# Performance work log

Measured on AMD Instinct MI355X. Metric: run time of the kernel, lower is better.

## Reference

```python
import jax, jax.numpy as jnp
import numpy as np

IOU_HI = 0.5
IOU_LO = 0.0
ROI_BS = 256
POS_RATIO = 0.25
BG = 20  # background class id; valid classes 0..BG-1
NUM_POS = int(ROI_BS * POS_RATIO)
DELTAS_SCALING = np.array([10.0, 10.0, 5.0, 5.0], dtype=np.float32)  # (x, y, w, h)


def _make_boxes(key, shape):
    ka, kb = jax.random.split(key)
    c = jax.random.uniform(ka, shape + (2,), minval=0.05, maxval=0.95)
    s = jax.random.uniform(kb, shape + (2,), minval=0.02, maxval=0.4)
    lo = jnp.clip(c - s / 2, 0.0, 1.0)
    hi = jnp.clip(c + s / 2, 0.0, 1.0)
    return jnp.concatenate([lo, hi], -1)  # (y1, x1, y2, x2), normalized


def setup_inputs() -> dict:
    key = jax.random.key(0)
    k1, k2, k3 = jax.random.split(key, 3)
    B, N, G = 32, 12000, 200
    rois = _make_boxes(k1, (B, N))
    gt_boxes = _make_boxes(k2, (B, G))
    # class == BG marks a padded / invalid GT box
    gt_class_ids = jax.random.randint(k3, (B, G), 0, BG + 1).astype(jnp.int32)
    return {"rois": rois, "gt_class_ids": gt_class_ids, "gt_boxes": gt_boxes}


def _iou(rois, gts):
    # rois [N,4], gts [G,4] in (y1,x1,y2,x2) -> [N,G]
    y1 = jnp.maximum(rois[:, None, 0], gts[None, :, 0])
    x1 = jnp.maximum(rois[:, None, 1], gts[None, :, 1])
    y2 = jnp.minimum(rois[:, None, 2], gts[None, :, 2])
    x2 = jnp.minimum(rois[:, None, 3], gts[None, :, 3])
    inter = jnp.clip(y2 - y1, 0.0) * jnp.clip(x2 - x1, 0.0)
    ar = (rois[:, 2] - rois[:, 0]) * (rois[:, 3] - rois[:, 1])
    ag = (gts[:, 2] - gts[:, 0]) * (gts[:, 3] - gts[:, 1])
    return inter / (ar[:, None] + ag[None, :] - inter + 1e-8)


def _encode(r, g):
    # (tx, ty, tw, th) * scaling, r/g: [K,4] in (y1,x1,y2,x2)
    eps = 1e-6
    rh = r[:, 2] - r[:, 0]; rw = r[:, 3] - r[:, 1]
    rcy = r[:, 0] + rh / 2; rcx = r[:, 1] + rw / 2
    gh = g[:, 2] - g[:, 0]; gw = g[:, 3] - g[:, 1]
    gcy = g[:, 0] + gh / 2; gcx = g[:, 1] + gw / 2
    tx = (gcx - rcx) / (rw + eps)
    ty = (gcy - rcy) / (rh + eps)
    tw = jnp.log(jnp.maximum(gw, eps) / (rw + eps))
    th = jnp.log(jnp.maximum(gh, eps) / (rh + eps))
    return jnp.stack([tx, ty, tw, th], -1) * jnp.asarray(DELTAS_SCALING)


def _per_image(rois, gt_cls, gt_boxes):
    iou = _iou(rois, gt_boxes)                       # [N,G]
    valid_gt = gt_cls < BG
    iou = jnp.where(valid_gt[None, :], iou, -1.0)
    max_iou = iou.max(1)                             # [N]
    best_gt = iou.argmax(1)                          # [N]
    pos = max_iou >= IOU_HI
    neg = (max_iou < IOU_HI) & (max_iou >= IOU_LO)

    # deterministic sampling: highest-IoU positives / negatives first
    pos_val, pos_idx = jax.lax.top_k(jnp.where(pos, max_iou, -1.0), NUM_POS)
    pos_ok = pos_val > 0.0
    neg_val, neg_idx = jax.lax.top_k(jnp.where(neg, max_iou + 2.0, -1.0), ROI_BS)
    neg_ok = neg_val > 0.0

    rP = jnp.arange(NUM_POS, dtype=jnp.float32)
    rN = jnp.arange(ROI_BS, dtype=jnp.float32)
    prio = jnp.concatenate([jnp.where(pos_ok, 1e9 - rP, -1e9 - rP),
                            jnp.where(neg_ok, 1e6 - rN, -1e6 - rN)])
    cand_idx = jnp.concatenate([pos_idx, neg_idx])
    cand_pos = jnp.concatenate([pos_ok, jnp.zeros(ROI_BS, bool)])
    _, sel = jax.lax.top_k(prio, ROI_BS)
    sel_roi = cand_idx[sel]                          # [ROI_BS]
    sel_is_pos = cand_pos[sel]                       # [ROI_BS]

    labels = jnp.where(sel_is_pos, gt_cls[best_gt[sel_roi]], BG)
    rois_sel = rois[sel_roi]                         # [ROI_BS,4]
    gts_sel = gt_boxes[best_gt[sel_roi]]             # [ROI_BS,4]
    t = _encode(rois_sel, gts_sel) * sel_is_pos[:, None].astype(rois.dtype)

    cls_onehot = jax.nn.one_hot(labels, BG + 1, dtype=rois.dtype)   # [ROI_BS,BG+1]
    onehot_fg = jax.nn.one_hot(labels, BG, dtype=rois.dtype)        # zero row for bg
    mask4 = jnp.repeat(onehot_fg, 4, axis=1)                        # [ROI_BS,4*BG]
    deltas_full = (onehot_fg[:, :, None] * t[:, None, :]).reshape(ROI_BS, 4 * BG)
    reg = jnp.concatenate([mask4, deltas_full], -1)                 # [ROI_BS,8*BG]
    return rois_sel, cls_onehot, reg


def reference(rois, gt_class_ids, gt_boxes):
    return jax.vmap(_per_image)(rois, gt_class_ids, gt_boxes)
```

## Files before the change

### kernel.cpp

```cpp
#include <hip/hip_runtime.h>
#include <stdint.h>

#pragma clang fp contract(off)

#define BATCH 32
#define NROI  12000
#define NGT   200
#define BGCLS 20
#define ROIBS 256
#define NPOS  64
#define NBIN  1024
#define CAP   2048
#define TSEL  1024
#define VPT2  12
#define HSH   16
#define HST   (NBIN + 2)
#define DELTA 1e-6f
#define RPT   2
#define IOBLK (256 * RPT)

__device__ __forceinline__ void roi_maxiou_all(const float4* cbox, const float* carea,
                                               int nv, float ry1, float rx1,
                                               float ry2, float rx2,
                                               float& best, int& bj) {
#pragma clang fp contract(off)
  float ar = (ry2 - ry1) * (rx2 - rx1);
  best = -1.0f; bj = 0;
#pragma unroll 4
  for (int j = 0; j < nv; ++j) {
    float4 q = cbox[j];
    float yy1 = fmaxf(ry1, q.x);
    float xx1 = fmaxf(rx1, q.y);
    float yy2 = fminf(ry2, q.z);
    float xx2 = fminf(rx2, q.w);
    float inter = fmaxf(yy2 - yy1, 0.0f) * fmaxf(xx2 - xx1, 0.0f);
    float den = ((ar + carea[j]) - inter) + 1e-8f;
    float iou = inter / den;
    if (iou > best) { best = iou; bj = j; }
  }
}

__device__ __forceinline__ float approx_max(const float4* cbox, const float* carea,
                                            int nv, float4 r) {
  float ar = (r.z - r.x) * (r.w - r.y);
  float va = -1.0f, vb = -1.0f;
#pragma unroll 4
  for (int j = 0; j < nv; ++j) {
    float4 q = cbox[j];
    float yy1 = fmaxf(r.x, q.x);
    float xx1 = fmaxf(r.y, q.y);
    float yy2 = fminf(r.z, q.z);
    float xx2 = fminf(r.w, q.w);
    float inter = fmaxf(yy2 - yy1, 0.0f) * fmaxf(xx2 - xx1, 0.0f);
    float den = ((ar + carea[j]) - inter) + 1e-8f;
    float a = inter * __builtin_amdgcn_rcpf(den);
    if (j & 1) vb = fmaxf(vb, a); else va = fmaxf(va, a);
  }
  return fmaxf(va, vb);
}

template <int NTHR>
__device__ __forceinline__ int stage_gt(float4* cbox, float* carea, int* ccls,
                                        int* snv, int* wtmp,
                                        const float* gtb, const int* gtc, int b) {
  const int tid = threadIdx.x;
  bool valid = false; float4 p = make_float4(0.f, 0.f, 0.f, 0.f); int cls = BGCLS;
  if (tid < NGT) {
    p = *(const float4*)(gtb + ((size_t)b * NGT + tid) * 4);
    cls = gtc[(size_t)b * NGT + tid];
    valid = (cls < BGCLS);
  }
  unsigned long long m = __ballot(valid);
  int w = tid >> 6;
  if ((tid & 63) == 0) wtmp[w] = __popcll(m);
  __syncthreads();
  if (tid == 0) {
    int s = 0;
    for (int i = 0; i < NTHR / 64; ++i) s += wtmp[i];
    *snv = s;
  }
  if (valid) {
    int off = 0;
    for (int i = 0; i < w; ++i) off += wtmp[i];
    int pos = off + __popcll(m & ((1ull << (tid & 63)) - 1ull));
    cbox[pos] = p;
    if (carea) carea[pos] = (p.z - p.x) * (p.w - p.y);
    if (ccls) ccls[pos] = cls;
  }
  __syncthreads();
  return *snv;
}

__global__ __launch_bounds__(256, 3) void k_ioumax(const float* __restrict__ rois,
                                                   const int* __restrict__ gtc,
                                                   const float* __restrict__ gtb,
                                                   float* __restrict__ max_iou) {
#pragma clang fp contract(off)
  __shared__ float4 cbox[NGT];
  __shared__ int snv, wtmp[4];
  const int b = blockIdx.y;
  const int tid = threadIdx.x;
  const int nv = stage_gt<256>(cbox, nullptr, nullptr, &snv, wtmp, gtb, gtc, b);

  const int n0 = blockIdx.x * IOBLK + tid;
  const int n1 = n0 + 256;
  const float4 r0 = (n0 < NROI)
      ? *(const float4*)(rois + ((size_t)b * NROI + n0) * 4)
      : make_float4(2.f, 2.f, 2.f, 2.f);
  const float4 r1 = (n1 < NROI)
      ? *(const float4*)(rois + ((size_t)b * NROI + n1) * 4)
      : make_float4(2.f, 2.f, 2.f, 2.f);
  const float ar0 = (r0.z - r0.x) * (r0.w - r0.y);
  const float ar1 = (r1.z - r1.x) * (r1.w - r1.y);
  float va0 = -1.0f, vb0 = -1.0f, va1 = -1.0f, vb1 = -1.0f;
#pragma unroll 4
  for (int j = 0; j < nv; ++j) {
    float4 q = cbox[j];
    float ag = (q.z - q.x) * (q.w - q.y);
    {
      float yy1 = fmaxf(r0.x, q.x);
      float xx1 = fmaxf(r0.y, q.y);
      float yy2 = fminf(r0.z, q.z);
      float xx2 = fminf(r0.w, q.w);
      float inter = fmaxf(yy2 - yy1, 0.0f) * fmaxf(xx2 - xx1, 0.0f);
      float den = ((ar0 + ag) - inter) + 1e-8f;
      float a = inter * __builtin_amdgcn_rcpf(den);
      if (j & 1) vb0 = fmaxf(vb0, a); else va0 = fmaxf(va0, a);
    }
    {
      float yy1 = fmaxf(r1.x, q.x);
      float xx1 = fmaxf(r1.y, q.y);
      float yy2 = fminf(r1.z, q.z);
      float xx2 = fminf(r1.w, q.w);
      float inter = fmaxf(yy2 - yy1, 0.0f) * fmaxf(xx2 - xx1, 0.0f);
      float den = ((ar1 + ag) - inter) + 1e-8f;
      float a = inter * __builtin_amdgcn_rcpf(den);
      if (j & 1) vb1 = fmaxf(vb1, a); else va1 = fmaxf(va1, a);
    }
  }
  if (n0 < NROI) max_iou[(size_t)b * NROI + n0] = fmaxf(va0, vb0);
  if (n1 < NROI) max_iou[(size_t)b * NROI + n1] = fmaxf(va1, vb1);
}

__global__ __launch_bounds__(TSEL) void k_selA(const float* __restrict__ rois,
                                               const int* __restrict__ gtc,
                                               const float* __restrict__ gtb,
                                               const float* __restrict__ mi,
                                               int* __restrict__ posCnt,
                                               int* __restrict__ posN,
                                               int* __restrict__ posBJ,
                                               int* __restrict__ negCnt,
                                               int* __restrict__ negN,
                                               int* __restrict__ negBJ) {
#pragma clang fp contract(off)
  __shared__ float4 cbox[NGT];
  __shared__ float carea[NGT];
  __shared__ int snv, wtmp[16];
  __shared__ int wtot[16], wnext[16];
  __shared__ int plist[CAP];
  __shared__ unsigned long long keyl[CAP];
  __shared__ int bjl[CAP];
  __shared__ int hs[HSH][HST];
  __shared__ int ss[NBIN];
  __shared__ int scnt, sX, sT, sOk;
  const int b = blockIdx.x >> 1;
  const bool isPos = (blockIdx.x & 1) == 0;
  const int tid = threadIdx.x;
  const int lane = tid & 63;
  const int nv = stage_gt<TSEL>(cbox, carea, nullptr, &snv, wtmp, gtb, gtc, b);

  float v[VPT2];
#pragma unroll
  for (int i = 0; i < VPT2; ++i) {
    int n = tid + (i << 10);
    v[i] = (n < NROI) ? mi[(size_t)b * NROI + n] : -3.0f;
  }

  auto mkbin = [](unsigned kh, unsigned base, int shift) -> int {
    int bin = ((int)(kh - base)) >> shift;
    return max(min(bin, NBIN - 1), 0);
  };
  const unsigned base = isPos ? 0x3F000000u : 0x40000000u;
  const int shift = isPos ? 13 : 11;

  for (int i = tid; i < HSH * HST; i += TSEL) ((int*)hs)[i] = 0;
  if (tid == 0) { scnt = 0; sX = 0; sOk = 0; }
  __syncthreads();
  const int sh = tid & (HSH - 1);
#pragma unroll
  for (int i = 0; i < VPT2; ++i) {
    int n = tid + (i << 10);
    float x = v[i];
    bool inb = isPos ? ((n < NROI) && (x >= 0.5f - DELTA))
                     : ((n < NROI) && (x < 0.5f + DELTA));
    if (inb) {
      unsigned kh = __float_as_uint(isPos ? x : (x + 2.0f));
      atomicAdd(&hs[sh][mkbin(kh, base, shift)], 1);
    }
    bool bnd = (n < NROI) && (x >= 0.5f - DELTA) && (x < 0.5f + DELTA);
    unsigned long long mx = __ballot(bnd);
    if (lane == 0 && mx) atomicAdd(&sX, __popcll(mx));
  }
  __syncthreads();
  const int limitWant = isPos ? NPOS : ROIBS;
  const int needv = limitWant + sX;

  {
    if (tid == 0) sT = 0;
    __syncthreads();
    int cnt_bin = 0;
#pragma unroll
    for (int i = 0; i < HSH; ++i) cnt_bin += hs[i][tid];
    const int w = tid >> 6;
    int sfx = cnt_bin;
#pragma unroll
    for (int off = 1; off < 64; off <<= 1) {
      int t = __shfl_down(sfx, off, 64);
      sfx += (lane + off < 64) ? t : 0;
    }
    if (lane == 0) wtot[w] = sfx;
    __syncthreads();
    if (tid < 16) {
      int s = 0;
      for (int i = tid + 1; i < 16; ++i) s += wtot[i];
      wnext[tid] = s;
    }
    __syncthreads();
    const int suffix = sfx + wnext[w];
    ss[tid] = suffix;
    __syncthreads();
    int nxt = (tid + 1 < NBIN) ? ss[tid + 1] : 0;
    if (suffix >= needv && nxt < needv) sT = tid;
    __syncthreads();
  }
  const int Tc = max(sT - 2, 0);

#pragma unroll
  for (int i = 0; i < VPT2; ++i) {
    int n = tid + (i << 10);
    float x = v[i];
    bool inb = isPos ? ((n < NROI) && (x >= 0.5f - DELTA))
                     : ((n < NROI) && (x < 0.5f + DELTA));
    bool pred = inb &&
        (mkbin(__float_as_uint(isPos ? x : (x + 2.0f)), base, shift) >= Tc);
    unsigned long long mk = __ballot(pred);
    int c = __popcll(mk);
    int bs = 0;
    if (lane == 0 && c) bs = atomicAdd(&scnt, c);
    bs = __shfl(bs, 0, 64);
    if (pred) {
      int idx = bs + __popcll(mk & ((1ull << lane) - 1ull));
      if (idx < CAP) plist[idx] = n;
    }
  }
  __syncthreads();
  const int cnt = min(scnt, CAP);

  for (int i = tid; i < cnt; i += TSEL) {
    int n = plist[i];
    const float4 r = *(const float4*)(rois + ((size_t)b * NROI + n) * 4);
    float best; int bj;
    roi_maxiou_all(cbox, carea, nv, r.x, r.y, r.z, r.w, best, bj);
    bool ok = isPos ? (best >= 0.5f) : (best < 0.5f);
    unsigned kh = __float_as_uint(isPos ? best : (best + 2.0f));
    keyl[i] = ok ? (((unsigned long long)kh << 32) | (unsigned)(0x7fffffff - n))
                 : 0ull;
    bjl[i] = bj;
    if (ok) atomicAdd(&sOk, 1);
  }
  __syncthreads();
  const int limit = min(sOk, limitWant);
  if (tid == 0) { if (isPos) posCnt[b] = limit; else negCnt[b] = limit; }

  int* dstN = isPos ? (posN + (size_t)b * NPOS) : (negN + (size_t)b * ROIBS);
  int* dstB = isPos ? (posBJ + (size_t)b * NPOS) : (negBJ + (size_t)b * ROIBS);
  for (int i = tid; i < cnt; i += TSEL) {
    unsigned long long ki = keyl[i];
    if (ki) {
      int r0 = 0, r1 = 0, r2 = 0, r3 = 0;
      int j = 0;
      for (; j + 4 <= cnt; j += 4) {
        r0 += (keyl[j + 0] > ki);
        r1 += (keyl[j + 1] > ki);
        r2 += (keyl[j + 2] > ki);
        r3 += (keyl[j + 3] > ki);
      }
      for (; j < cnt; ++j) r0 += (keyl[j] > ki);
      int rank = r0 + r1 + r2 + r3;
      if (rank < limit) {
        dstN[rank] = 0x7fffffff - (int)(ki & 0xffffffffu);
        dstB[rank] = bjl[i];
      }
    }
  }
}

__global__ __launch_bounds__(TSEL) void k_emit(const float* __restrict__ rois,
                                               const int* __restrict__ gtc,
                                               const float* __restrict__ gtb,
                                               const int* __restrict__ posCnt,
                                               const int* __restrict__ posN,
                                               const int* __restrict__ posBJ,
                                               const int* __restrict__ negCnt,
                                               const int* __restrict__ negN,
                                               const int* __restrict__ negBJ,
                                               float* __restrict__ out) {
#pragma clang fp contract(off)
  __shared__ float4 cbox[NGT];
  __shared__ float carea[NGT];
  __shared__ int ccls[NGT];
  __shared__ int snv, wtmp[16];
  const int b = blockIdx.x;
  const int tid = threadIdx.x;
  stage_gt<TSEL>(cbox, carea, ccls, &snv, wtmp, gtb, gtc, b);

  const int P = min(posCnt[b], NPOS);
  const int NC = negCnt[b];
  const int slot = tid >> 2, q = tid & 3;
  int r = 0, bj = 0, isp = 0;
  if (slot < P) {
    r = posN[(size_t)b * NPOS + slot];
    bj = posBJ[(size_t)b * NPOS + slot];
    isp = 1;
  } else {
    int j = slot - P;
    if (j < NC) {
      r = negN[(size_t)b * ROIBS + j];
      bj = negBJ[(size_t)b * ROIBS + j];
    }
  }
  const float4 rv = *(const float4*)(rois + ((size_t)b * NROI + r) * 4);
  float ry1 = rv.x, rx1 = rv.y, ry2 = rv.z, rx2 = rv.w;
  int label = isp ? ccls[bj] : BGCLS;

  float* out1 = out;
  float* out2 = out + (size_t)BATCH * ROIBS * 4;
  float* out3 = out + (size_t)BATCH * ROIBS * 25;
  size_t row = (size_t)b * ROIBS + slot;

  if (q == 0) {
    *(float4*)(out1 + row * 4) = rv;
    float* o2 = out2 + row * 21;
    for (int c = 0; c <= BGCLS; ++c) o2[c] = (c == label) ? 1.0f : 0.0f;
  }

  float t0 = 0.f, t1 = 0.f, t2 = 0.f, t3 = 0.f;
  if (isp) {
    const float eps = 1e-6f;
    float4 g = cbox[bj];
    float rh = ry2 - ry1, rw = rx2 - rx1;
    float rcy = ry1 + rh * 0.5f, rcx = rx1 + rw * 0.5f;
    float gh = g.z - g.x, gw = g.w - g.y;
    float gcy = g.x + gh * 0.5f, gcx = g.y + gw * 0.5f;
    t0 = ((gcx - rcx) / (rw + eps)) * 10.0f;
    t1 = ((gcy - rcy) / (rh + eps)) * 10.0f;
    t2 = logf(fmaxf(gw, eps) / (rw + eps)) * 5.0f;
    t3 = logf(fmaxf(gh, eps) / (rh + eps)) * 5.0f;
  }
  int m0 = label * 4;
  float* o3 = out3 + row * 160;
  for (int c = q * 10; c < q * 10 + 10; ++c) {
    float4 wv = make_float4(0.f, 0.f, 0.f, 0.f);
    if (isp) {
      float* wp = &wv.x;
#pragma unroll
      for (int jj = 0; jj < 4; ++jj) {
        int e = c * 4 + jj;
        float x = 0.f;
        if (e >= m0 && e < m0 + 4) x = 1.0f;
        int d = e - 80 - m0;
        if (d == 0) x = t0; else if (d == 1) x = t1;
        else if (d == 2) x = t2; else if (d == 3) x = t3;
        wp[jj] = x;
      }
    }
    *(float4*)(o3 + c * 4) = wv;
  }
}

__global__ __launch_bounds__(TSEL) void k_sel_mono(const float* __restrict__ rois,
                                                   const int* __restrict__ gtc,
                                                   const float* __restrict__ gtb,
                                                   float* __restrict__ out) {
#pragma clang fp contract(off)
  __shared__ float4 cbox[NGT];
  __shared__ float carea[NGT];
  __shared__ int ccls[NGT];
  __shared__ int snv, wtmp[16];
  __shared__ int wtot[16], wnext[16];
  __shared__ int plist[CAP];
  __shared__ unsigned long long keyl[CAP];
  __shared__ int bjl[CAP];
  __shared__ int hs[HSH][HST];
  __shared__ int ss[NBIN];
  __shared__ int sel_r[ROIBS];
  __shared__ int sel_b[ROIBS];
  __shared__ int scnt, sX, sT, sPos;
  const int b = blockIdx.x;
  const int tid = threadIdx.x;
  const int lane = tid & 63;
  if (tid < ROIBS) { sel_r[tid] = 0; sel_b[tid] = 0; }
  const int nv = stage_gt<TSEL>(cbox, carea, ccls, &snv, wtmp, gtb, gtc, b);

  float v[VPT2];
#pragma unroll
  for (int i = 0; i < VPT2; ++i) {
    int n = tid + (i << 10);
    if (n < NROI) {
      const float4 r = *(const float4*)(rois + ((size_t)b * NROI + n) * 4);
      v[i] = approx_max(cbox, carea, nv, r);
    } else v[i] = -3.0f;
  }

  auto mkbin = [](unsigned kh, unsigned base, int shift) -> int {
    int bin = ((int)(kh - base)) >> shift;
    return max(min(bin, NBIN - 1), 0);
  };
  auto find_T = [&](int needv) -> int {
    if (tid == 0) sT = 0;
    __syncthreads();
    int cnt_bin = 0;
#pragma unroll
    for (int i = 0; i < HSH; ++i) cnt_bin += hs[i][tid];
    const int w = tid >> 6;
    int sfx = cnt_bin;
#pragma unroll
    for (int off = 1; off < 64; off <<= 1) {
      int t = __shfl_down(sfx, off, 64);
      sfx += (lane + off < 64) ? t : 0;
    }
    if (lane == 0) wtot[w] = sfx;
    __syncthreads();
    if (tid < 16) {
      int s = 0;
      for (int i = tid + 1; i < 16; ++i) s += wtot[i];
      wnext[tid] = s;
    }
    __syncthreads();
    const int suffix = sfx + wnext[w];
    ss[tid] = suffix;
    __syncthreads();
    int nxt = (tid + 1 < NBIN) ? ss[tid + 1] : 0;
    if (suffix >= needv && nxt < needv) sT = tid;
    __syncthreads();
    return sT;
  };
  auto rank_of = [&](unsigned long long ki, int cnt) -> int {
    int r0 = 0, r1 = 0, r2 = 0, r3 = 0;
    int j = 0;
    for (; j + 4 <= cnt; j += 4) {
      r0 += (keyl[j + 0] > ki);
      r1 += (keyl[j + 1] > ki);
      r2 += (keyl[j + 2] > ki);
      r3 += (keyl[j + 3] > ki);
    }
    for (; j < cnt; ++j) r0 += (keyl[j] > ki);
    return r0 + r1 + r2 + r3;
  };
  const int sh = tid & (HSH - 1);

  for (int i = tid; i < HSH * HST; i += TSEL) ((int*)hs)[i] = 0;
  if (tid == 0) { scnt = 0; sX = 0; sPos = 0; }
  __syncthreads();
#pragma unroll
  for (int i = 0; i < VPT2; ++i) {
    int n = tid + (i << 10);
    float x = v[i];
    bool inb = (n < NROI) && (x >= 0.5f - DELTA);
    if (inb) atomicAdd(&hs[sh][mkbin(__float_as_uint(x), 0x3F000000u, 13)], 1);
    bool bnd = inb && (x < 0.5f + DELTA);
    unsigned long long mx = __ballot(bnd);
    if (lane == 0 && mx) atomicAdd(&sX, __popcll(mx));
  }
  __syncthreads();
  const int XB = sX;
  const int Tp = max(find_T(NPOS + XB) - 2, 0);
#pragma unroll
  for (int i = 0; i < VPT2; ++i) {
    int n = tid + (i << 10);
    float x = v[i];
    bool pred = (n < NROI) && (x >= 0.5f - DELTA) &&
                (mkbin(__float_as_uint(x), 0x3F000000u, 13) >= Tp);
    unsigned long long mk = __ballot(pred);
    int c = __popcll(mk);
    int bs = 0;
    if (lane == 0 && c) bs = atomicAdd(&scnt, c);
    bs = __shfl(bs, 0, 64);
    if (pred) {
      int idx = bs + __popcll(mk & ((1ull << lane) - 1ull));
      if (idx < CAP) plist[idx] = n;
    }
  }
  __syncthreads();
  const int cntp = min(scnt, CAP);
  for (int i = tid; i < cntp; i += TSEL) {
    int n = plist[i];
    const float4 r = *(const float4*)(rois + ((size_t)b * NROI + n) * 4);
    float best; int bj;
    roi_maxiou_all(cbox, carea, nv, r.x, r.y, r.z, r.w, best, bj);
    bool ok = (best >= 0.5f);
    keyl[i] = ok ? (((unsigned long long)__float_as_uint(best) << 32)
                   | (unsigned)(0x7fffffff - n)) : 0ull;
    bjl[i] = bj;
    if (ok) atomicAdd(&sPos, 1);
  }
  __syncthreads();
  const int P = min(sPos, NPOS);
  for (int i = tid; i < cntp; i += TSEL) {
    unsigned long long ki = keyl[i];
    if (ki) {
      int rank = rank_of(ki, cntp);
      if (rank < P) {
        sel_r[rank] = 0x7fffffff - (int)(ki & 0xffffffffu);
        sel_b[rank] = bjl[i];
      }
    }
  }
  __syncthreads();

  const int need = ROIBS - P;
  for (int i = tid; i < HSH * HST; i += TSEL) ((int*)hs)[i] = 0;
  if (tid == 0) scnt = 0;
  __syncthreads();
#pragma unroll
  for (int i = 0; i < VPT2; ++i) {
    int n = tid + (i << 10);
    float x = v[i];
    if (n < NROI && x < 0.5f + DELTA)
      atomicAdd(&hs[sh][mkbin(__float_as_uint(x + 2.0f), 0x40000000u, 11)], 1);
  }
  __syncthreads();
  const int Tn = max(find_T(need + XB) - 2, 0);
#pragma unroll
  for (int i = 0; i < VPT2; ++i) {
    int n = tid + (i << 10);
    float x = v[i];
    bool pred = (n < NROI) && (x < 0.5f + DELTA) &&
                (mkbin(__float_as_uint(x + 2.0f), 0x40000000u, 11) >= Tn);
    unsigned long long mk = __ballot(pred);
    int c = __popcll(mk);
    int bs = 0;
    if (lane == 0 && c) bs = atomicAdd(&scnt, c);
    bs = __shfl(bs, 0, 64);
    if (pred) {
      int idx = bs + __popcll(mk & ((1ull << lane) - 1ull));
      if (idx < CAP) plist[idx] = n;
    }
  }
  __syncthreads();
  const int cntn = min(scnt, CAP);
  for (int i = tid; i < cntn; i += TSEL) {
    int n = plist[i];
    const float4 r = *(const float4*)(rois + ((size_t)b * NROI + n) * 4);
    float best; int bj;
    roi_maxiou_all(cbox, carea, nv, r.x, r.y, r.z, r.w, best, bj);
    bool ok = (best < 0.5f);
    keyl[i] = ok ? (((unsigned long long)__float_as_uint(best + 2.0f) << 32)
                   | (unsigned)(0x7fffffff - n)) : 0ull;
    bjl[i] = bj;
  }
  __syncthreads();
  for (int i = tid; i < cntn; i += TSEL) {
    unsigned long long ki = keyl[i];
    if (ki) {
      int rank = rank_of(ki, cntn);
      if (rank < need) {
        sel_r[P + rank] = 0x7fffffff - (int)(ki & 0xffffffffu);
        sel_b[P + rank] = bjl[i];
      }
    }
  }
  __syncthreads();

  {
    const int slot = tid >> 2, q = tid & 3;
    const int r = sel_r[slot];
    const int bj = sel_b[slot];
    const int isp = (slot < P) ? 1 : 0;
    const float4 rv = *(const float4*)(rois + ((size_t)b * NROI + r) * 4);
    float ry1 = rv.x, rx1 = rv.y, ry2 = rv.z, rx2 = rv.w;
    int label = isp ? ccls[bj] : BGCLS;
    float* out1 = out;
    float* out2 = out + (size_t)BATCH * ROIBS * 4;
    float* out3 = out + (size_t)BATCH * ROIBS * 25;
    size_t row = (size_t)b * ROIBS + slot;
    if (q == 0) {
      *(float4*)(out1 + row * 4) = rv;
      float* o2 = out2 + row * 21;
      for (int c = 0; c <= BGCLS; ++c) o2[c] = (c == label) ? 1.0f : 0.0f;
    }
    float t0 = 0.f, t1 = 0.f, t2 = 0.f, t3 = 0.f;
    if (isp) {
      const float eps = 1e-6f;
      float4 g = cbox[bj];
      float rh = ry2 - ry1, rw = rx2 - rx1;
      float rcy = ry1 + rh * 0.5f, rcx = rx1 + rw * 0.5f;
      float gh = g.z - g.x, gw = g.w - g.y;
      float gcy = g.x + gh * 0.5f, gcx = g.y + gw * 0.5f;
      t0 = ((gcx - rcx) / (rw + eps)) * 10.0f;
      t1 = ((gcy - rcy) / (rh + eps)) * 10.0f;
      t2 = logf(fmaxf(gw, eps) / (rw + eps)) * 5.0f;
      t3 = logf(fmaxf(gh, eps) / (rh + eps)) * 5.0f;
    }
    int m0 = label * 4;
    float* o3 = out3 + row * 160;
    for (int c = q * 10; c < q * 10 + 10; ++c) {
      float4 wv = make_float4(0.f, 0.f, 0.f, 0.f);
      if (isp) {
        float* wp = &wv.x;
#pragma unroll
        for (int jj = 0; jj < 4; ++jj) {
          int e = c * 4 + jj;
          float x = 0.f;
          if (e >= m0 && e < m0 + 4) x = 1.0f;
          int d = e - 80 - m0;
          if (d == 0) x = t0; else if (d == 1) x = t1;
          else if (d == 2) x = t2; else if (d == 3) x = t3;
          wp[jj] = x;
        }
      }
      *(float4*)(o3 + c * 4) = wv;
    }
  }
}

extern "C" void kernel_launch(void* const* d_in, const int* in_sizes, int n_in,
                              void* d_out, int out_size, void* d_ws, size_t ws_size,
                              hipStream_t stream) {
  const float* rois = (const float*)d_in[0];
  const int*   gtc  = (const int*)d_in[1];
  const float* gtb  = (const float*)d_in[2];
  float*       out  = (float*)d_out;

  const size_t A = (size_t)BATCH * NROI;
  const size_t nint = 32 + (size_t)BATCH * NPOS * 2 + 32 + (size_t)BATCH * ROIBS * 2;
  const size_t need = (A + nint) * 4;
  if (d_ws && ws_size >= need) {
    float* mi = (float*)d_ws;
    int* p = (int*)((float*)d_ws + A);
    int* posCnt = p;             p += 32;
    int* posN   = p;             p += BATCH * NPOS;
    int* posBJ  = p;             p += BATCH * NPOS;
    int* negCnt = p;             p += 32;
    int* negN   = p;             p += BATCH * ROIBS;
    int* negBJ  = p;
    k_ioumax<<<dim3((NROI + IOBLK - 1) / IOBLK, BATCH), 256, 0, stream>>>(rois, gtc, gtb, mi);
    k_selA<<<BATCH * 2, TSEL, 0, stream>>>(rois, gtc, gtb, mi,
                                           posCnt, posN, posBJ,
                                           negCnt, negN, negBJ);
    k_emit<<<BATCH, TSEL, 0, stream>>>(rois, gtc, gtb, posCnt, posN, posBJ,
                                       negCnt, negN, negBJ, out);
  } else {
    k_sel_mono<<<BATCH, TSEL, 0, stream>>>(rois, gtc, gtb, out);
  }
}
```

Before: 88.27 us.

## Fuse emit into selection kernel with negative blocks computing positive count themselves

Removes the separate emit kernel. Each pos/neg selection block now writes its own output rows directly. Negative blocks work out the positive count P on their own so they know where their slots start: they count ROIs clearly above threshold and run an exact IoU recheck on boundary ROIs. This drops one launch and a round trip through global memory, in exchange for extra redundant work and more shared memory in the negative blocks. The fminf/fmaxf calls are also replaced with compare-select helpers in the IoU loop.

```diff
diff --git a/kernel.cpp b/kernel.cpp
--- a/kernel.cpp
+++ b/kernel.cpp
@@ -11,6 +11,7 @@
 #define NPOS  64
 #define NBIN  1024
 #define CAP   2048
+#define BCAP  256
 #define TSEL  1024
 #define VPT2  12
 #define HSH   16
@@ -40,25 +41,6 @@
   }
 }
 
-__device__ __forceinline__ float approx_max(const float4* cbox, const float* carea,
-                                            int nv, float4 r) {
-  float ar = (r.z - r.x) * (r.w - r.y);
-  float va = -1.0f, vb = -1.0f;
-#pragma unroll 4
-  for (int j = 0; j < nv; ++j) {
-    float4 q = cbox[j];
-    float yy1 = fmaxf(r.x, q.x);
-    float xx1 = fmaxf(r.y, q.y);
-    float yy2 = fminf(r.z, q.z);
-    float xx2 = fminf(r.w, q.w);
-    float inter = fmaxf(yy2 - yy1, 0.0f) * fmaxf(xx2 - xx1, 0.0f);
-    float den = ((ar + carea[j]) - inter) + 1e-8f;
-    float a = inter * __builtin_amdgcn_rcpf(den);
-    if (j & 1) vb = fmaxf(vb, a); else va = fmaxf(va, a);
-  }
-  return fmaxf(va, vb);
-}
-
 template <int NTHR>
 __device__ __forceinline__ int stage_gt(float4* cbox, float* carea, int* ccls,
                                         int* snv, int* wtmp,
@@ -90,6 +72,9 @@
   __syncthreads();
   return *snv;
 }
+
+__device__ __forceinline__ float tmax(float a, float b) { return a > b ? a : b; }
+__device__ __forceinline__ float tmin(float a, float b) { return a < b ? a : b; }
 
 __global__ __launch_bounds__(256, 3) void k_ioumax(const float* __restrict__ rois,
                                                    const int* __restrict__ gtc,
@@ -118,43 +103,41 @@
     float4 q = cbox[j];
     float ag = (q.z - q.x) * (q.w - q.y);
     {
-      float yy1 = fmaxf(r0.x, q.x);
-      float xx1 = fmaxf(r0.y, q.y);
-      float yy2 = fminf(r0.z, q.z);
-      float xx2 = fminf(r0.w, q.w);
-      float inter = fmaxf(yy2 - yy1, 0.0f) * fmaxf(xx2 - xx1, 0.0f);
+      float yy1 = tmax(r0.x, q.x);
+      float xx1 = tmax(r0.y, q.y);
+      float yy2 = tmin(r0.z, q.z);
+      float xx2 = tmin(r0.w, q.w);
+      float dy = yy2 - yy1, dx = xx2 - xx1;
+      float inter = tmax(dy, 0.0f) * tmax(dx, 0.0f);
       float den = ((ar0 + ag) - inter) + 1e-8f;
       float a = inter * __builtin_amdgcn_rcpf(den);
-      if (j & 1) vb0 = fmaxf(vb0, a); else va0 = fmaxf(va0, a);
+      if (j & 1) vb0 = tmax(vb0, a); else va0 = tmax(va0, a);
     }
     {
-      float yy1 = fmaxf(r1.x, q.x);
-      float xx1 = fmaxf(r1.y, q.y);
-      float yy2 = fminf(r1.z, q.z);
-      float xx2 = fminf(r1.w, q.w);
-      float inter = fmaxf(yy2 - yy1, 0.0f) * fmaxf(xx2 - xx1, 0.0f);
+      float yy1 = tmax(r1.x, q.x);
+      float xx1 = tmax(r1.y, q.y);
+      float yy2 = tmin(r1.z, q.z);
+      float xx2 = tmin(r1.w, q.w);
+      float dy = yy2 - yy1, dx = xx2 - xx1;
+      float inter = tmax(dy, 0.0f) * tmax(dx, 0.0f);
       float den = ((ar1 + ag) - inter) + 1e-8f;
       float a = inter * __builtin_amdgcn_rcpf(den);
-      if (j & 1) vb1 = fmaxf(vb1, a); else va1 = fmaxf(va1, a);
-    }
-  }
-  if (n0 < NROI) max_iou[(size_t)b * NROI + n0] = fmaxf(va0, vb0);
-  if (n1 < NROI) max_iou[(size_t)b * NROI + n1] = fmaxf(va1, vb1);
+      if (j & 1) vb1 = tmax(vb1, a); else va1 = tmax(va1, a);
+    }
+  }
+  if (n0 < NROI) max_iou[(size_t)b * NROI + n0] = tmax(va0, vb0);
+  if (n1 < NROI) max_iou[(size_t)b * NROI + n1] = tmax(va1, vb1);
 }
 
-__global__ __launch_bounds__(TSEL) void k_selA(const float* __restrict__ rois,
-                                               const int* __restrict__ gtc,
-                                               const float* __restrict__ gtb,
-                                               const float* __restrict__ mi,
-                                               int* __restrict__ posCnt,
-                                               int* __restrict__ posN,
-                                               int* __restrict__ posBJ,
-                                               int* __restrict__ negCnt,
-                                               int* __restrict__ negN,
-                                               int* __restrict__ negBJ) {
+__global__ __launch_bounds__(TSEL) void k_selAB(const float* __restrict__ rois,
+                                                const int* __restrict__ gtc,
+                                                const float* __restrict__ gtb,
+                                                const float* __restrict__ mi,
+                                                float* __restrict__ out) {
 #pragma clang fp contract(off)
   __shared__ float4 cbox[NGT];
   __shared__ float carea[NGT];
+  __shared__ int ccls[NGT];
   __shared__ int snv, wtmp[16];
   __shared__ int wtot[16], wnext[16];
   __shared__ int plist[CAP];
@@ -162,12 +145,15 @@
   __shared__ int bjl[CAP];
   __shared__ int hs[HSH][HST];
   __shared__ int ss[NBIN];
-  __shared__ int scnt, sX, sT, sOk;
+  __shared__ int selN[ROIBS];
+  __shared__ int selB[ROIBS];
+  __shared__ int blist[BCAP];
+  __shared__ int scnt, sX, sT, sOk, sC1, sC2, sBn;
   const int b = blockIdx.x >> 1;
   const bool isPos = (blockIdx.x & 1) == 0;
   const int tid = threadIdx.x;
   const int lane = tid & 63;
-  const int nv = stage_gt<TSEL>(cbox, carea, nullptr, &snv, wtmp, gtb, gtc, b);
+  const int nv = stage_gt<TSEL>(cbox, carea, ccls, &snv, wtmp, gtb, gtc, b);
 
   float v[VPT2];
 #pragma unroll
@@ -184,7 +170,8 @@
   const int shift = isPos ? 13 : 11;
 
   for (int i = tid; i < HSH * HST; i += TSEL) ((int*)hs)[i] = 0;
-  if (tid == 0) { scnt = 0; sX = 0; sOk = 0; }
+  if (tid < ROIBS) { selN[tid] = 0; selB[tid] = 0; }
+  if (tid == 0) { scnt = 0; sX = 0; sOk = 0; sC1 = 0; sC2 = 0; sBn = 0; }
   __syncthreads();
   const int sh = tid & (HSH - 1);
 #pragma unroll
@@ -200,9 +187,31 @@
     bool bnd = (n < NROI) && (x >= 0.5f - DELTA) && (x < 0.5f + DELTA);
     unsigned long long mx = __ballot(bnd);
     if (lane == 0 && mx) atomicAdd(&sX, __popcll(mx));
-  }
-  __syncthreads();
-  const int limitWant = isPos ? NPOS : ROIBS;
+    if (!isPos) {
+      if (bnd) {
+        int bi = atomicAdd(&sBn, 1);
+        if (bi < BCAP) blist[bi] = n;
+      }
+      unsigned long long mc = __ballot((n < NROI) && (x >= 0.5f + DELTA));
+      if (lane == 0 && mc) atomicAdd(&sC1, __popcll(mc));
+    }
+  }
+  __syncthreads();
+
+  int P = 0;
+  if (!isPos) {
+    int bn = min(sBn, BCAP);
+    for (int i = tid; i < bn; i += TSEL) {
+      int n = blist[i];
+      const float4 r = *(const float4*)(rois + ((size_t)b * NROI + n) * 4);
+      float best; int bj;
+      roi_maxiou_all(cbox, carea, nv, r.x, r.y, r.z, r.w, best, bj);
+      if (best >= 0.5f) atomicAdd(&sC2, 1);
+    }
+    __syncthreads();
+    P = min(sC1 + sC2, NPOS);
+  }
+  const int limitWant = isPos ? NPOS : (ROIBS - P);
   const int needv = limitWant + sX;
 
   {
@@ -269,11 +278,9 @@
     if (ok) atomicAdd(&sOk, 1);
   }
   __syncthreads();
-  const int limit = min(sOk, limitWant);
-  if (tid == 0) { if (isPos) posCnt[b] = limit; else negCnt[b] = limit; }
-
-  int* dstN = isPos ? (posN + (size_t)b * NPOS) : (negN + (size_t)b * ROIBS);
-  int* dstB = isPos ? (posBJ + (size_t)b * NPOS) : (negBJ + (size_t)b * ROIBS);
+  if (isPos) P = min(sOk, NPOS);
+  const int limit = isPos ? P : (ROIBS - P);
+
   for (int i = tid; i < cnt; i += TSEL) {
     unsigned long long ki = keyl[i];
     if (ki) {
@@ -288,94 +295,89 @@
       for (; j < cnt; ++j) r0 += (keyl[j] > ki);
       int rank = r0 + r1 + r2 + r3;
       if (rank < limit) {
-        dstN[rank] = 0x7fffffff - (int)(ki & 0xffffffffu);
-        dstB[rank] = bjl[i];
+        selN[rank] = 0x7fffffff - (int)(ki & 0xffffffffu);
+        selB[rank] = bjl[i];
+      }
+    }
+  }
+  __syncthreads();
+
+  {
+    const int sl = tid >> 2, q = tid & 3;
+    const int slot = isPos ? sl : (P + sl);
+    const bool live = isPos ? (slot < P) : (slot < ROIBS);
+    if (live) {
+      const int r = selN[sl];
+      const int bj = selB[sl];
+      const int isp = isPos ? 1 : 0;
+      const float4 rv = *(const float4*)(rois + ((size_t)b * NROI + r) * 4);
+      float ry1 = rv.x, rx1 = rv.y, ry2 = rv.z, rx2 = rv.w;
+      int label = isp ? ccls[bj] : BGCLS;
+
+      float* out1 = out;
+      float* out2 = out + (size_t)BATCH * ROIBS * 4;
+      float* out3 = out + (size_t)BATCH * ROIBS * 25;
+      size_t row = (size_t)b * ROIBS + slot;
+
+      if (q == 0) {
+        *(float4*)(out1 + row * 4) = rv;
+        float* o2 = out2 + row * 21;
+        for (int c = 0; c <= BGCLS; ++c) o2[c] = (c == label) ? 1.0f : 0.0f;
+      }
+
+      float t0 = 0.f, t1 = 0.f, t2 = 0.f, t3 = 0.f;
+      if (isp) {
+        const float eps = 1e-6f;
+        float4 g = cbox[bj];
+        float rh = ry2 - ry1, rw = rx2 - rx1;
+        float rcy = ry1 + rh * 0.5f, rcx = rx1 + rw * 0.5f;
+        float gh = g.z - g.x, gw = g.w - g.y;
+        float gcy = g.x + gh * 0.5f, gcx = g.y + gw * 0.5f;
+        t0 = ((gcx - rcx) / (rw + eps)) * 10.0f;
+        t1 = ((gcy - rcy) / (rh + eps)) * 10.0f;
+        t2 = logf(fmaxf(gw, eps) / (rw + eps)) * 5.0f;
+        t3 = logf(fmaxf(gh, eps) / (rh + eps)) * 5.0f;
+      }
+      int m0 = label * 4;
+      float* o3 = out3 + row * 160;
+      for (int c = q * 10; c < q * 10 + 10; ++c) {
+        float4 wv = make_float4(0.f, 0.f, 0.f, 0.f);
+        if (isp) {
+          float* wp = &wv.x;
+#pragma unroll
+          for (int jj = 0; jj < 4; ++jj) {
+            int e = c * 4 + jj;
+            float x = 0.f;
+            if (e >= m0 && e < m0 + 4) x = 1.0f;
+            int d = e - 80 - m0;
+            if (d == 0) x = t0; else if (d == 1) x = t1;
+            else if (d == 2) x = t2; else if (d == 3) x = t3;
+            wp[jj] = x;
+          }
+        }
+        *(float4*)(o3 + c * 4) = wv;
       }
     }
   }
 }
 
-__global__ __launch_bounds__(TSEL) void k_emit(const float* __restrict__ rois,
-                                               const int* __restrict__ gtc,
-                                               const float* __restrict__ gtb,
-                                               const int* __restrict__ posCnt,
-                                               const int* __restrict__ posN,
-                                               const int* __restrict__ posBJ,
-                                               const int* __restrict__ negCnt,
-                                               const int* __restrict__ negN,
-                                               const int* __restrict__ negBJ,
-                                               float* __restrict__ out) {
-#pragma clang fp contract(off)
-  __shared__ float4 cbox[NGT];
-  __shared__ float carea[NGT];
-  __shared__ int ccls[NGT];
-  __shared__ int snv, wtmp[16];
-  const int b = blockIdx.x;
-  const int tid = threadIdx.x;
-  stage_gt<TSEL>(cbox, carea, ccls, &snv, wtmp, gtb, gtc, b);
-
-  const int P = min(posCnt[b], NPOS);
-  const int NC = negCnt[b];
-  const int slot = tid >> 2, q = tid & 3;
-  int r = 0, bj = 0, isp = 0;
-  if (slot < P) {
-    r = posN[(size_t)b * NPOS + slot];
-    bj = posBJ[(size_t)b * NPOS + slot];
-    isp = 1;
-  } else {
-    int j = slot - P;
-    if (j < NC) {
-      r = negN[(size_t)b * ROIBS + j];
-      bj = negBJ[(size_t)b * ROIBS + j];
-    }
-  }
-  const float4 rv = *(const float4*)(rois + ((size_t)b * NROI + r) * 4);
-  float ry1 = rv.x, rx1 = rv.y, ry2 = rv.z, rx2 = rv.w;
-  int label = isp ? ccls[bj] : BGCLS;
-
-  float* out1 = out;
-  float* out2 = out + (size_t)BATCH * ROIBS * 4;
-  float* out3 = out + (size_t)BATCH * ROIBS * 25;
-  size_t row = (size_t)b * ROIBS + slot;
-
-  if (q == 0) {
-    *(float4*)(out1 + row * 4) = rv;
-    float* o2 = out2 + row * 21;
-    for (int c = 0; c <= BGCLS; ++c) o2[c] = (c == label) ? 1.0f : 0.0f;
-  }
-
-  float t0 = 0.f, t1 = 0.f, t2 = 0.f, t3 = 0.f;
-  if (isp) {
-    const float eps = 1e-6f;
-    float4 g = cbox[bj];
-    float rh = ry2 - ry1, rw = rx2 - rx1;
-    float rcy = ry1 + rh * 0.5f, rcx = rx1 + rw * 0.5f;
-    float gh = g.z - g.x, gw = g.w - g.y;
-    float gcy = g.x + gh * 0.5f, gcx = g.y + gw * 0.5f;
-    t0 = ((gcx - rcx) / (rw + eps)) * 10.0f;
-    t1 = ((gcy - rcy) / (rh + eps)) * 10.0f;
-    t2 = logf(fmaxf(gw, eps) / (rw + eps)) * 5.0f;
-    t3 = logf(fmaxf(gh, eps) / (rh + eps)) * 5.0f;
-  }
-  int m0 = label * 4;
-  float* o3 = out3 + row * 160;
-  for (int c = q * 10; c < q * 10 + 10; ++c) {
-    float4 wv = make_float4(0.f, 0.f, 0.f, 0.f);
-    if (isp) {
-      float* wp = &wv.x;
-#pragma unroll
-      for (int jj = 0; jj < 4; ++jj) {
-        int e = c * 4 + jj;
-        float x = 0.f;
-        if (e >= m0 && e < m0 + 4) x = 1.0f;
-        int d = e - 80 - m0;
-        if (d == 0) x = t0; else if (d == 1) x = t1;
-        else if (d == 2) x = t2; else if (d == 3) x = t3;
-        wp[jj] = x;
-      }
-    }
-    *(float4*)(o3 + c * 4) = wv;
-  }
+__device__ __forceinline__ float approx_max_f(const float4* cbox, const float* carea,
+                                              int nv, float4 r) {
+  float ar = (r.z - r.x) * (r.w - r.y);
+  float va = -1.0f, vb = -1.0f;
+#pragma unroll 4
+  for (int j = 0; j < nv; ++j) {
+    float4 q = cbox[j];
+    float yy1 = tmax(r.x, q.x);
+    float xx1 = tmax(r.y, q.y);
+    float yy2 = tmin(r.z, q.z);
+    float xx2 = tmin(r.w, q.w);
+    float inter = tmax(yy2 - yy1, 0.0f) * tmax(xx2 - xx1, 0.0f);
+    float den = ((ar + carea[j]) - inter) + 1e-8f;
+    float a = inter * __builtin_amdgcn_rcpf(den);
+    if (j & 1) vb = tmax(vb, a); else va = tmax(va, a);
+  }
+  return tmax(va, vb);
 }
 
 __global__ __launch_bounds__(TSEL) void k_sel_mono(const float* __restrict__ rois,
@@ -408,7 +410,7 @@
     int n = tid + (i << 10);
     if (n < NROI) {
       const float4 r = *(const float4*)(rois + ((size_t)b * NROI + n) * 4);
-      v[i] = approx_max(cbox, carea, nv, r);
+      v[i] = approx_max_f(cbox, carea, nv, r);
     } else v[i] = -3.0f;
   }
 
@@ -632,24 +634,11 @@
   const float* gtb  = (const float*)d_in[2];
   float*       out  = (float*)d_out;
 
-  const size_t A = (size_t)BATCH * NROI;
-  const size_t nint = 32 + (size_t)BATCH * NPOS * 2 + 32 + (size_t)BATCH * ROIBS * 2;
-  const size_t need = (A + nint) * 4;
+  const size_t need = (size_t)BATCH * NROI * sizeof(float);
   if (d_ws && ws_size >= need) {
     float* mi = (float*)d_ws;
-    int* p = (int*)((float*)d_ws + A);
-    int* posCnt = p;             p += 32;
-    int* posN   = p;             p += BATCH * NPOS;
-    int* posBJ  = p;             p += BATCH * NPOS;
-    int* negCnt = p;             p += 32;
-    int* negN   = p;             p += BATCH * ROIBS;
-    int* negBJ  = p;
     k_ioumax<<<dim3((NROI + IOBLK - 1) / IOBLK, BATCH), 256, 0, stream>>>(rois, gtc, gtb, mi);
-    k_selA<<<BATCH * 2, TSEL, 0, stream>>>(rois, gtc, gtb, mi,
-                                           posCnt, posN, posBJ,
-                                           negCnt, negN, negBJ);
-    k_emit<<<BATCH, TSEL, 0, stream>>>(rois, gtc, gtb, posCnt, posN, posBJ,
-                                       negCnt, negN, negBJ, out);
+    k_selAB<<<BATCH * 2, TSEL, 0, stream>>>(rois, gtc, gtb, mi, out);
   } else {
     k_sel_mono<<<BATCH, TSEL, 0, stream>>>(rois, gtc, gtb, out);
   }
```

Result: slower. 100.4 us (+13.7%).
